# Kernel optimization log

Measured on AMD Instinct MI355X. Metric: run time of the kernel, lower is better.

The kernel has to match this reference:

```python
import jax, jax.numpy as jnp
import numpy as np

B, S, E, H = 2, 2048, 1024, 16
D = E // H  # head dim = 64
ROPE_BASE = 10000.0


def _rope(x):
    # x: [B, H, S, D]; interleaved-pair rotary embeddings (torchtune style)
    d2 = D // 2
    theta = 1.0 / (ROPE_BASE ** (jnp.arange(d2, dtype=jnp.float32) * 2.0 / D))  # [D/2]
    pos = jnp.arange(S, dtype=jnp.float32)
    ang = pos[:, None] * theta[None, :]            # [S, D/2]
    cos, sin = jnp.cos(ang), jnp.sin(ang)          # broadcast over B,H
    xr = x.reshape(B, H, S, d2, 2)
    x1, x2 = xr[..., 0], xr[..., 1]
    o1 = x1 * cos - x2 * sin
    o2 = x1 * sin + x2 * cos
    return jnp.stack([o1, o2], axis=-1).reshape(B, H, S, D)


def setup_inputs() -> dict:
    key = jax.random.key(0)
    ks = jax.random.split(key, 5)
    scale = 1.0 / np.sqrt(E)
    return {
        "x": jax.random.normal(ks[0], (B, S, E), dtype=jnp.float32),
        "Wq": jax.random.normal(ks[1], (E, E), dtype=jnp.float32) * scale,
        "Wk": jax.random.normal(ks[2], (E, E), dtype=jnp.float32) * scale,
        "Wv": jax.random.normal(ks[3], (E, E), dtype=jnp.float32) * scale,
        "Wo": jax.random.normal(ks[4], (E, E), dtype=jnp.float32) * scale,
    }


def reference(x, Wq, Wk, Wv, Wo):
    # torch Linear: y = x @ W^T
    def proj(W):
        return (x @ W.T).reshape(B, S, H, D).transpose(0, 2, 1, 3)  # [B,H,S,D]

    q = _rope(proj(Wq))
    k = _rope(proj(Wk))
    v = proj(Wv)

    attn_scale = 1.0 / np.sqrt(E)  # faithful: scales by sqrt(d_embed), not head dim
    scores = jnp.einsum('bhqd,bhkd->bhqk', q, k) * attn_scale  # [B,H,S,S]
    causal = jnp.tril(jnp.ones((S, S), dtype=bool))
    scores = jnp.where(causal, scores, -jnp.inf)
    probs = jax.nn.softmax(scores, axis=-1)
    out = jnp.einsum('bhqk,bhkd->bhqd', probs, v)  # [B,H,S,D]
    out = out.transpose(0, 2, 1, 3).reshape(B, S, E)
    return out @ Wo.T
```

## Files before the change

kernel.cpp:

```cpp
#include <hip/hip_runtime.h>
#include <hip/hip_bf16.h>
#include <math.h>

typedef __bf16 bf16;
typedef __bf16 bf16x8 __attribute__((ext_vector_type(8)));
typedef float f32x4 __attribute__((ext_vector_type(4)));

#define SEQ 2048
#define EMB 1024
#define NH  16
#define HD  64
#define NROWS 4096

#define GLOAD_LDS16(gp, lp)                                             \
    __builtin_amdgcn_global_load_lds(                                   \
        (const __attribute__((address_space(1))) void*)(gp),            \
        (__attribute__((address_space(3))) void*)(lp), 16, 0, 0)

__global__ __launch_bounds__(256) void cvt_rope_kernel(
    const float* __restrict__ x,  const float* __restrict__ Wq,
    const float* __restrict__ Wk, const float* __restrict__ Wv,
    const float* __restrict__ Wo,
    bf16* __restrict__ xb, bf16* __restrict__ Wqb, bf16* __restrict__ Wkb,
    bf16* __restrict__ Wvb, bf16* __restrict__ Wob,
    float* __restrict__ ctab, float* __restrict__ stab)
{
    int b = blockIdx.x;
    if (b >= 4096) {
        int t = (b - 4096) * 256 + threadIdx.x;
        int s = t >> 5;
        int j = t & 31;
        double freq = pow(10000.0, -(double)j / 32.0);
        double ang = (double)s * freq;
        ctab[t] = (float)cos(ang);
        stab[t] = (float)sin(ang);
        return;
    }
    const float* src; bf16* dst; int boff;
    if      (b < 2048) { src = x;  dst = xb;  boff = b;        }
    else if (b < 2560) { src = Wq; dst = Wqb; boff = b - 2048; }
    else if (b < 3072) { src = Wk; dst = Wkb; boff = b - 2560; }
    else if (b < 3584) { src = Wv; dst = Wvb; boff = b - 3072; }
    else               { src = Wo; dst = Wob; boff = b - 3584; }
    size_t off = (size_t)boff * 2048 + (size_t)threadIdx.x * 8;
    float4 f0 = *(const float4*)(src + off);
    float4 f1 = *(const float4*)(src + off + 4);
    bf16x8 v;
    v[0] = (bf16)f0.x; v[1] = (bf16)f0.y; v[2] = (bf16)f0.z; v[3] = (bf16)f0.w;
    v[4] = (bf16)f1.x; v[5] = (bf16)f1.y; v[6] = (bf16)f1.z; v[7] = (bf16)f1.w;
    *(bf16x8*)(dst + off) = v;
}

__global__ __launch_bounds__(256) void qkv_rope_kernel(
    const bf16* __restrict__ x,
    const bf16* __restrict__ Wq, const bf16* __restrict__ Wk, const bf16* __restrict__ Wv,
    const float* __restrict__ ctab, const float* __restrict__ stab,
    bf16* __restrict__ q_ws, bf16* __restrict__ kf_ws, bf16* __restrict__ vf_ws)
{
    __shared__ __align__(16) bf16 SMEM[24576];

    const int t    = threadIdx.x;
    const int lane = t & 63;
    const int wave = t >> 6;
    const int col  = lane & 15;
    const int quad = lane >> 4;

    const int nblk = blockIdx.x;
    const int m0   = blockIdx.y * 128;

    const bf16* W; int nloc;
    if (nblk < 8)       { W = Wq; nloc = nblk * 128; }
    else if (nblk < 16) { W = Wk; nloc = (nblk - 8) * 128; }
    else                { W = Wv; nloc = (nblk - 16) * 128; }

    const bf16 *ga[2], *gb[2];
#pragma unroll
    for (int j = 0; j < 2; j++) {
        int c = t + j * 256;
        ga[j] = x + (size_t)(m0 + (c >> 2)) * EMB + (c & 3) * 8;
        gb[j] = W + (size_t)(nloc + (c >> 2)) * EMB + (c & 3) * 8;
    }

    const int wm = (wave >> 1) * 64;
    const int wn = (wave & 1) * 64;

    f32x4 acc[4][4];
#pragma unroll
    for (int i = 0; i < 4; i++)
#pragma unroll
        for (int j = 0; j < 4; j++) acc[i][j] = (f32x4){0.f, 0.f, 0.f, 0.f};

    auto stage = [&](int kt, int b) {
        bf16* As_ = SMEM + b * 8192;
        bf16* Bs_ = As_ + 4096;
        const int kc = kt * 32;
#pragma unroll
        for (int j = 0; j < 2; j++) {
            const int c = t + j * 256;
            GLOAD_LDS16(ga[j] + kc, As_ + c * 8);
            GLOAD_LDS16(gb[j] + kc, Bs_ + c * 8);
        }
    };
    auto compute = [&](int b) {
        bf16* As_ = SMEM + b * 8192;
        bf16* Bs_ = As_ + 4096;
        bf16x8 a[4], bb[4];
#pragma unroll
        for (int mt = 0; mt < 4; mt++)
            a[mt] = *(const bf16x8*)(As_ + (wm + mt * 16 + col) * 32 + quad * 8);
#pragma unroll
        for (int nt = 0; nt < 4; nt++)
            bb[nt] = *(const bf16x8*)(Bs_ + (wn + nt * 16 + col) * 32 + quad * 8);
#pragma unroll
        for (int mt = 0; mt < 4; mt++)
#pragma unroll
            for (int nt = 0; nt < 4; nt++)
                acc[mt][nt] = __builtin_amdgcn_mfma_f32_16x16x32_bf16(a[mt], bb[nt], acc[mt][nt], 0, 0, 0);
    };

    stage(0, 0);
    stage(1, 1);
    int b = 0;
    for (int kt = 0; kt < 31; kt++) {
        asm volatile("s_waitcnt vmcnt(4)\n\ts_barrier" ::: "memory");
        if (kt < 30) stage(kt + 2, (kt + 2) % 3);
        compute(b);
        b = (b == 2) ? 0 : b + 1;
    }
    asm volatile("s_waitcnt vmcnt(0)\n\ts_barrier" ::: "memory");
    compute(b);
    __syncthreads();

    bf16* Es = SMEM + wave * 4608;

    const int n0w  = nblk * 128 + wn;
    const int m0w  = m0 + wm;
    const int bb_  = m0w >> 11;
    const int ss0  = m0w & (SEQ - 1);
    const int h    = (n0w >> 6) & 15;
    const int bh   = bb_ * NH + h;
    const int kind = (n0w < 1024) ? 0 : (n0w < 2048 ? 1 : 2);

#pragma unroll
    for (int mt = 0; mt < 4; mt++) {
#pragma unroll
        for (int nt = 0; nt < 4; nt++) {
            const int d  = nt * 16 + col;
            const int jj = d >> 1;
#pragma unroll
            for (int r = 0; r < 4; r++) {
                const int ss_l = mt * 16 + quad * 4 + r;
                float v = acc[mt][nt][r];
                if (kind < 2) {
                    float partner = __shfl_xor(v, 1, 64);
                    float c  = ctab[(ss0 + ss_l) * 32 + jj];
                    float sn = stab[(ss0 + ss_l) * 32 + jj];
                    float o = ((d & 1) == 0) ? (v * c - partner * sn)
                                             : (partner * sn + v * c);
                    if (kind == 0) {
                        Es[ss_l * 72 + d] = (bf16)(o * 0.03125f);
                    } else {
                        int eoff = ((ss_l >> 4) * 2 + (d >> 5)) * 512
                                 + ((d >> 3) & 3) * 128 + (ss_l & 15) * 8 + (d & 7);
                        Es[eoff] = (bf16)o;
                    }
                } else {
                    int eoff = ((ss_l >> 5) * 4 + (d >> 4)) * 512
                             + ((ss_l >> 3) & 3) * 128 + (d & 15) * 8 + (ss_l & 7);
                    Es[eoff] = (bf16)v;
                }
            }
        }
    }

    const int row = lane >> 3, c8 = lane & 7;
    if (kind == 0) {
        bf16* qbase = q_ws + ((size_t)bh * SEQ + ss0) * HD;
#pragma unroll
        for (int i = 0; i < 8; i++) {
            bf16x8 vv = *(const bf16x8*)&Es[(i * 8 + row) * 72 + c8 * 8];
            *(bf16x8*)(qbase + (size_t)(i * 8 + row) * HD + c8 * 8) = vv;
        }
    } else if (kind == 1) {
        bf16* kbase = kf_ws + ((size_t)bh * 128 + (ss0 >> 4)) * 1024;
#pragma unroll
        for (int i = 0; i < 8; i++) {
            bf16x8 vv = *(const bf16x8*)&Es[i * 512 + lane * 8];
            *(bf16x8*)(kbase + i * 512 + lane * 8) = vv;
        }
    } else {
        bf16* vbase = vf_ws + ((size_t)bh * 64 + (ss0 >> 5)) * 2048;
#pragma unroll
        for (int i = 0; i < 8; i++) {
            bf16x8 vv = *(const bf16x8*)&Es[i * 512 + lane * 8];
            *(bf16x8*)(vbase + i * 512 + lane * 8) = vv;
        }
    }
}

__global__ __launch_bounds__(128) void attn_kernel(
    const bf16* __restrict__ q_ws, const bf16* __restrict__ kf,
    const bf16* __restrict__ vf, bf16* __restrict__ attn_ws)
{
    __shared__ float comb_o[2][4][4][64];
    __shared__ float comb_l[2][64];

    const int lane = threadIdx.x & 63;
    const int wave = threadIdx.x >> 6;
    const int col  = lane & 15;
    const int quad = lane >> 4;

    const int qt = 63 - (int)(blockIdx.x >> 5);
    const int bh = blockIdx.x & 31;
    const int b_ = bh >> 4;
    const int h  = bh & 15;
    const int qb = qt * 32;
    const int nk = qt + 1;

    const bf16* Q  = q_ws + (size_t)bh * SEQ * HD;
    const bf16* Kf = kf + (size_t)bh * 131072;
    const bf16* Vf = vf + (size_t)bh * 131072;

    bf16x8 aq[2][2];
#pragma unroll
    for (int f = 0; f < 2; f++) {
        const bf16* qp = Q + (size_t)(qb + f * 16 + col) * HD + quad * 8;
        aq[f][0] = *(const bf16x8*)(qp);
        aq[f][1] = *(const bf16x8*)(qp + 32);
    }

    f32x4 acc_o[2][4];
#pragma unroll
    for (int f = 0; f < 2; f++)
#pragma unroll
        for (int i = 0; i < 4; i++) acc_o[f][i] = (f32x4){0.f, 0.f, 0.f, 0.f};
    float lsum[2] = {0.f, 0.f};

    int psrc[8];
#pragma unroll
    for (int j = 0; j < 8; j++)
        psrc[j] = ((((quad * 2 + (j >> 2)) & 3) << 4) | col) << 2;

    int s0 = (wave < nk) ? wave : 0;
    bf16x8 Ka[2][2], nKa[2][2];
    {
        const bf16* p = Kf + (size_t)s0 * 2048 + lane * 8;
        Ka[0][0] = *(const bf16x8*)(p);
        Ka[0][1] = *(const bf16x8*)(p + 512);
        Ka[1][0] = *(const bf16x8*)(p + 1024);
        Ka[1][1] = *(const bf16x8*)(p + 1536);
    }

    for (int s = wave; s < nk; s += 2) {
        bf16x8 Vb[4];
        {
            const bf16* p = Vf + (size_t)s * 2048 + lane * 8;
            Vb[0] = *(const bf16x8*)(p);
            Vb[1] = *(const bf16x8*)(p + 512);
            Vb[2] = *(const bf16x8*)(p + 1024);
            Vb[3] = *(const bf16x8*)(p + 1536);
        }

        f32x4 sT[2][2];
        __builtin_amdgcn_s_setprio(1);
#pragma unroll
        for (int g = 0; g < 2; g++)
#pragma unroll
            for (int f = 0; f < 2; f++) {
                f32x4 z = (f32x4){0.f, 0.f, 0.f, 0.f};
                z = __builtin_amdgcn_mfma_f32_16x16x32_bf16(Ka[g][0], aq[f][0], z, 0, 0, 0);
                z = __builtin_amdgcn_mfma_f32_16x16x32_bf16(Ka[g][1], aq[f][1], z, 0, 0, 0);
                sT[g][f] = z;
            }
        __builtin_amdgcn_s_setprio(0);

        {
            int sn = (s + 2 < nk) ? s + 2 : s;
            const bf16* p = Kf + (size_t)sn * 2048 + lane * 8;
            nKa[0][0] = *(const bf16x8*)(p);
            nKa[0][1] = *(const bf16x8*)(p + 512);
            nKa[1][0] = *(const bf16x8*)(p + 1024);
            nKa[1][1] = *(const bf16x8*)(p + 1536);
        }

        float p[2][2][4];
        if (s == nk - 1) {
#pragma unroll
            for (int g = 0; g < 2; g++)
#pragma unroll
                for (int f = 0; f < 2; f++) {
                    const int qg = qb + f * 16 + col;
#pragma unroll
                    for (int r = 0; r < 4; r++) {
                        int key = s * 32 + g * 16 + quad * 4 + r;
                        float e = (key <= qg) ? __expf(sT[g][f][r]) : 0.f;
                        p[g][f][r] = e;
                        lsum[f] += e;
                    }
                }
        } else {
#pragma unroll
            for (int g = 0; g < 2; g++)
#pragma unroll
                for (int f = 0; f < 2; f++)
#pragma unroll
                    for (int r = 0; r < 4; r++) {
                        float e = __expf(sT[g][f][r]);
                        p[g][f][r] = e;
                        lsum[f] += e;
                    }
        }

#pragma unroll
        for (int f = 0; f < 2; f++) {
            unsigned int pk[4];
#pragma unroll
            for (int r = 0; r < 4; r++) {
                unsigned int lo = __builtin_bit_cast(unsigned short, (bf16)p[0][f][r]);
                unsigned int hi = __builtin_bit_cast(unsigned short, (bf16)p[1][f][r]);
                pk[r] = (hi << 16) | lo;
            }
            bf16x8 a_p;
#pragma unroll
            for (int j = 0; j < 8; j++) {
                unsigned int g = (unsigned int)__builtin_amdgcn_ds_bpermute(psrc[j], (int)pk[j & 3]);
                unsigned short bits = (quad < 2) ? (unsigned short)(g & 0xffff)
                                                 : (unsigned short)(g >> 16);
                a_p[j] = __builtin_bit_cast(bf16, bits);
            }
            __builtin_amdgcn_s_setprio(1);
#pragma unroll
            for (int nt = 0; nt < 4; nt++)
                acc_o[f][nt] = __builtin_amdgcn_mfma_f32_16x16x32_bf16(a_p, Vb[nt], acc_o[f][nt], 0, 0, 0);
            __builtin_amdgcn_s_setprio(0);
        }

        Ka[0][0] = nKa[0][0]; Ka[0][1] = nKa[0][1];
        Ka[1][0] = nKa[1][0]; Ka[1][1] = nKa[1][1];
    }

    if (wave == 1) {
#pragma unroll
        for (int f = 0; f < 2; f++) {
            comb_l[f][lane] = lsum[f];
#pragma unroll
            for (int nt = 0; nt < 4; nt++)
#pragma unroll
                for (int r = 0; r < 4; r++)
                    comb_o[f][nt][r][lane] = acc_o[f][nt][r];
        }
    }
    __syncthreads();

    if (wave == 0) {
#pragma unroll
        for (int f = 0; f < 2; f++) {
            lsum[f] += comb_l[f][lane];
#pragma unroll
            for (int nt = 0; nt < 4; nt++)
#pragma unroll
                for (int r = 0; r < 4; r++)
                    acc_o[f][nt][r] += comb_o[f][nt][r][lane];
        }

#pragma unroll
        for (int f = 0; f < 2; f++) {
            lsum[f] += __shfl_xor(lsum[f], 16, 64);
            lsum[f] += __shfl_xor(lsum[f], 32, 64);
        }
#pragma unroll
        for (int f = 0; f < 2; f++)
#pragma unroll
            for (int r = 0; r < 4; r++) {
                float l_r = __shfl(lsum[f], quad * 4 + r, 64);
                float inv = 1.0f / l_r;
                int q = qb + f * 16 + quad * 4 + r;
                bf16* orow = attn_ws + (size_t)(b_ * SEQ + q) * EMB + h * HD;
#pragma unroll
                for (int nt = 0; nt < 4; nt++)
                    orow[nt * 16 + col] = (bf16)(acc_o[f][nt][r] * inv);
            }
    }
}

__global__ __launch_bounds__(256) void oproj_kernel(
    const bf16* __restrict__ attn_ws, const bf16* __restrict__ Wo,
    float* __restrict__ out)
{
    __shared__ __align__(16) bf16 SMEM[24576];

    const int t    = threadIdx.x;
    const int lane = t & 63;
    const int wave = t >> 6;
    const int col  = lane & 15;
    const int quad = lane >> 4;

    const int n0 = blockIdx.x * 128;
    const int m0 = blockIdx.y * 128;

    const bf16 *ga[2], *gb[2];
#pragma unroll
    for (int j = 0; j < 2; j++) {
        int c = t + j * 256;
        ga[j] = attn_ws + (size_t)(m0 + (c >> 2)) * EMB + (c & 3) * 8;
        gb[j] = Wo + (size_t)(n0 + (c >> 2)) * EMB + (c & 3) * 8;
    }

    const int wm = (wave >> 1) * 64;
    const int wn = (wave & 1) * 64;

    f32x4 acc[4][4];
#pragma unroll
    for (int i = 0; i < 4; i++)
#pragma unroll
        for (int j = 0; j < 4; j++) acc[i][j] = (f32x4){0.f, 0.f, 0.f, 0.f};

    auto stage = [&](int kt, int b) {
        bf16* As_ = SMEM + b * 8192;
        bf16* Bs_ = As_ + 4096;
        const int kc = kt * 32;
#pragma unroll
        for (int j = 0; j < 2; j++) {
            const int c = t + j * 256;
            GLOAD_LDS16(ga[j] + kc, As_ + c * 8);
            GLOAD_LDS16(gb[j] + kc, Bs_ + c * 8);
        }
    };
    auto compute = [&](int b) {
        bf16* As_ = SMEM + b * 8192;
        bf16* Bs_ = As_ + 4096;
        bf16x8 a[4], bb[4];
#pragma unroll
        for (int mt = 0; mt < 4; mt++)
            a[mt] = *(const bf16x8*)(As_ + (wm + mt * 16 + col) * 32 + quad * 8);
#pragma unroll
        for (int nt = 0; nt < 4; nt++)
            bb[nt] = *(const bf16x8*)(Bs_ + (wn + nt * 16 + col) * 32 + quad * 8);
#pragma unroll
        for (int mt = 0; mt < 4; mt++)
#pragma unroll
            for (int nt = 0; nt < 4; nt++)
                acc[mt][nt] = __builtin_amdgcn_mfma_f32_16x16x32_bf16(a[mt], bb[nt], acc[mt][nt], 0, 0, 0);
    };

    stage(0, 0);
    stage(1, 1);
    int b = 0;
    for (int kt = 0; kt < 31; kt++) {
        asm volatile("s_waitcnt vmcnt(4)\n\ts_barrier" ::: "memory");
        if (kt < 30) stage(kt + 2, (kt + 2) % 3);
        compute(b);
        b = (b == 2) ? 0 : b + 1;
    }
    asm volatile("s_waitcnt vmcnt(0)\n\ts_barrier" ::: "memory");
    compute(b);
    __syncthreads();

    float* Os = (float*)SMEM + (size_t)wave * 2304;
    const int row = lane >> 3, c8 = lane & 7;
    float* obase = out + (size_t)(m0 + wm) * EMB + n0 + wn;
#pragma unroll
    for (int p = 0; p < 2; p++) {
#pragma unroll
        for (int mt = 0; mt < 4; mt++)
#pragma unroll
            for (int ntl = 0; ntl < 2; ntl++)
#pragma unroll
                for (int r = 0; r < 4; r++)
                    Os[(mt * 16 + quad * 4 + r) * 36 + ntl * 16 + col] = acc[mt][p * 2 + ntl][r];
#pragma unroll
        for (int i = 0; i < 8; i++) {
            float4 vv = *(const float4*)&Os[(i * 8 + row) * 36 + c8 * 4];
            *(float4*)(obase + (size_t)(i * 8 + row) * EMB + p * 32 + c8 * 4) = vv;
        }
    }
}

extern "C" void kernel_launch(void* const* d_in, const int* in_sizes, int n_in,
                              void* d_out, int out_size, void* d_ws, size_t ws_size,
                              hipStream_t stream) {
    const float* x  = (const float*)d_in[0];
    const float* Wq = (const float*)d_in[1];
    const float* Wk = (const float*)d_in[2];
    const float* Wv = (const float*)d_in[3];
    const float* Wo = (const float*)d_in[4];
    float* out = (float*)d_out;

    char* ws = (char*)d_ws;
    bf16* q_ws    = (bf16*)(ws);
    bf16* kf_ws   = (bf16*)(ws + (8u  << 20));
    bf16* vf_ws   = (bf16*)(ws + (16u << 20));
    bf16* xb      = (bf16*)(ws + (24u << 20));
    bf16* attn_ws = (bf16*)(ws + (24u << 20));
    bf16* Wqb     = (bf16*)(ws + (32u << 20));
    bf16* Wkb     = (bf16*)(ws + (34u << 20));
    bf16* Wvb     = (bf16*)(ws + (36u << 20));
    bf16* Wob     = (bf16*)(ws + (38u << 20));
    float* ctab   = (float*)(ws + (40u << 20));
    float* stab   = ctab + SEQ * 32;

    hipLaunchKernelGGL(cvt_rope_kernel, dim3(4352), dim3(256), 0, stream,
                       x, Wq, Wk, Wv, Wo, xb, Wqb, Wkb, Wvb, Wob, ctab, stab);
    hipLaunchKernelGGL(qkv_rope_kernel, dim3(24, 32), dim3(256), 0, stream,
                       xb, Wqb, Wkb, Wvb, ctab, stab, q_ws, kf_ws, vf_ws);
    hipLaunchKernelGGL(attn_kernel, dim3(2048), dim3(128), 0, stream,
                       q_ws, kf_ws, vf_ws, attn_ws);
    hipLaunchKernelGGL(oproj_kernel, dim3(8, 32), dim3(256), 0, stream,
                       attn_ws, Wob, out);
}
```

Before: 175.6 us.

## Retile QKV GEMM to 256x256 blocks with 8 waves and swizzled LDS

The QKV projection GEMM moves from 128x128 tiles with 4 waves and a triple-buffered K=32 pipeline to 256x256 tiles with 8 waves, a double-buffered K=64 pipeline and an XOR-swizzled LDS layout. The B-tile loads are interleaved into four compute phases, and s_setprio raises wave priority around the MFMA bursts. The goal is more data reuse per LDS load, fewer LDS bank conflicts and better overlap of loads with compute. In exchange, the grid shrinks to 192 blocks, which may underfill the GPU, and register and LDS pressure rise (128KB LDS per block).

```diff
diff --git a/kernel.cpp b/kernel.cpp
--- a/kernel.cpp
+++ b/kernel.cpp
@@ -51,149 +51,177 @@
     *(bf16x8*)(dst + off) = v;
 }
 
-__global__ __launch_bounds__(256) void qkv_rope_kernel(
+__global__ __launch_bounds__(512, 2) void qkv_rope_kernel(
     const bf16* __restrict__ x,
     const bf16* __restrict__ Wq, const bf16* __restrict__ Wk, const bf16* __restrict__ Wv,
     const float* __restrict__ ctab, const float* __restrict__ stab,
     bf16* __restrict__ q_ws, bf16* __restrict__ kf_ws, bf16* __restrict__ vf_ws)
 {
-    __shared__ __align__(16) bf16 SMEM[24576];
+    __shared__ __align__(16) bf16 SMEM[65536];
 
     const int t    = threadIdx.x;
     const int lane = t & 63;
     const int wave = t >> 6;
     const int col  = lane & 15;
     const int quad = lane >> 4;
+    const int wmi  = wave >> 2;
+    const int wni  = wave & 3;
 
     const int nblk = blockIdx.x;
-    const int m0   = blockIdx.y * 128;
-
-    const bf16* W; int nloc;
-    if (nblk < 8)       { W = Wq; nloc = nblk * 128; }
-    else if (nblk < 16) { W = Wk; nloc = (nblk - 8) * 128; }
-    else                { W = Wv; nloc = (nblk - 16) * 128; }
-
-    const bf16 *ga[2], *gb[2];
-#pragma unroll
-    for (int j = 0; j < 2; j++) {
-        int c = t + j * 256;
-        ga[j] = x + (size_t)(m0 + (c >> 2)) * EMB + (c & 3) * 8;
-        gb[j] = W + (size_t)(nloc + (c >> 2)) * EMB + (c & 3) * 8;
-    }
-
-    const int wm = (wave >> 1) * 64;
-    const int wn = (wave & 1) * 64;
-
-    f32x4 acc[4][4];
-#pragma unroll
-    for (int i = 0; i < 4; i++)
+    const int m0   = blockIdx.y * 256;
+
+    const bf16* W;
+    const int nloc = (nblk & 3) * 256;
+    if (nblk < 4)      W = Wq;
+    else if (nblk < 8) W = Wk;
+    else               W = Wv;
+
+    const int srow = t >> 3;
+    const int scol = ((t & 7) ^ (srow & 7)) * 8;
+    const bf16* gaA = x + (size_t)(m0   + srow) * EMB + scol;
+    const bf16* gaB = W + (size_t)(nloc + srow) * EMB + scol;
+
+    f32x4 acc[8][4];
+#pragma unroll
+    for (int i = 0; i < 8; i++)
 #pragma unroll
         for (int j = 0; j < 4; j++) acc[i][j] = (f32x4){0.f, 0.f, 0.f, 0.f};
 
-    auto stage = [&](int kt, int b) {
-        bf16* As_ = SMEM + b * 8192;
-        bf16* Bs_ = As_ + 4096;
-        const int kc = kt * 32;
-#pragma unroll
-        for (int j = 0; j < 2; j++) {
-            const int c = t + j * 256;
-            GLOAD_LDS16(ga[j] + kc, As_ + c * 8);
-            GLOAD_LDS16(gb[j] + kc, Bs_ + c * 8);
-        }
+    auto stageA = [&](int kt, int h) {
+        bf16* dst = SMEM + (kt & 1) * 32768 + h * 8192 + t * 8;
+        const bf16* src = gaA + (size_t)(h * 128) * EMB + kt * 64;
+        GLOAD_LDS16(src,            dst);
+        GLOAD_LDS16(src + 64 * EMB, dst + 4096);
     };
-    auto compute = [&](int b) {
-        bf16* As_ = SMEM + b * 8192;
-        bf16* Bs_ = As_ + 4096;
-        bf16x8 a[4], bb[4];
-#pragma unroll
-        for (int mt = 0; mt < 4; mt++)
-            a[mt] = *(const bf16x8*)(As_ + (wm + mt * 16 + col) * 32 + quad * 8);
-#pragma unroll
-        for (int nt = 0; nt < 4; nt++)
-            bb[nt] = *(const bf16x8*)(Bs_ + (wn + nt * 16 + col) * 32 + quad * 8);
-#pragma unroll
-        for (int mt = 0; mt < 4; mt++)
-#pragma unroll
-            for (int nt = 0; nt < 4; nt++)
-                acc[mt][nt] = __builtin_amdgcn_mfma_f32_16x16x32_bf16(a[mt], bb[nt], acc[mt][nt], 0, 0, 0);
+    auto stageB = [&](int kt, int h) {
+        bf16* dst = SMEM + (kt & 1) * 32768 + 16384 + h * 8192 + t * 8;
+        const bf16* src = gaB + (size_t)(h * 128) * EMB + kt * 64;
+        GLOAD_LDS16(src,            dst);
+        GLOAD_LDS16(src + 64 * EMB, dst + 4096);
     };
 
-    stage(0, 0);
-    stage(1, 1);
-    int b = 0;
-    for (int kt = 0; kt < 31; kt++) {
-        asm volatile("s_waitcnt vmcnt(4)\n\ts_barrier" ::: "memory");
-        if (kt < 30) stage(kt + 2, (kt + 2) % 3);
-        compute(b);
-        b = (b == 2) ? 0 : b + 1;
-    }
-    asm volatile("s_waitcnt vmcnt(0)\n\ts_barrier" ::: "memory");
-    compute(b);
+    const int swz = (col & 7) << 3;
+
+    auto phase = [&](int p, int mh, int nh, int skt, int sh) {
+        const bf16* Ab = SMEM + p * 32768;
+        const bf16* Bb = SMEM + p * 32768 + 16384;
+        bf16x8 a[4][2], b[2][2];
+#pragma unroll
+        for (int mtl = 0; mtl < 4; mtl++) {
+            const int row = wmi * 128 + mh * 64 + mtl * 16 + col;
+#pragma unroll
+            for (int kk = 0; kk < 2; kk++)
+                a[mtl][kk] = *(const bf16x8*)(Ab + row * 64 + ((quad * 8 + kk * 32) ^ swz));
+        }
+#pragma unroll
+        for (int ntl = 0; ntl < 2; ntl++) {
+            const int row = wni * 64 + nh * 32 + ntl * 16 + col;
+#pragma unroll
+            for (int kk = 0; kk < 2; kk++)
+                b[ntl][kk] = *(const bf16x8*)(Bb + row * 64 + ((quad * 8 + kk * 32) ^ swz));
+        }
+        if (skt >= 0) stageB(skt, sh);
+        __builtin_amdgcn_s_setprio(1);
+#pragma unroll
+        for (int mtl = 0; mtl < 4; mtl++)
+#pragma unroll
+            for (int ntl = 0; ntl < 2; ntl++) {
+                f32x4 c = acc[mh * 4 + mtl][nh * 2 + ntl];
+                c = __builtin_amdgcn_mfma_f32_16x16x32_bf16(a[mtl][0], b[ntl][0], c, 0, 0, 0);
+                c = __builtin_amdgcn_mfma_f32_16x16x32_bf16(a[mtl][1], b[ntl][1], c, 0, 0, 0);
+                acc[mh * 4 + mtl][nh * 2 + ntl] = c;
+            }
+        __builtin_amdgcn_s_setprio(0);
+        __builtin_amdgcn_s_barrier();
+    };
+
+    stageA(0, 0); stageA(0, 1); stageB(0, 0); stageB(0, 1);
+
+    for (int kt = 0; kt < 15; kt++) {
+        const int p = kt & 1;
+        stageA(kt + 1, 0); stageA(kt + 1, 1);
+        asm volatile("s_waitcnt vmcnt(4)" ::: "memory");
+        __builtin_amdgcn_s_barrier();
+        phase(p, 0, 0, kt + 1, 0);
+        phase(p, 0, 1, kt + 1, 1);
+        phase(p, 1, 0, -1, 0);
+        phase(p, 1, 1, -1, 0);
+    }
+    asm volatile("s_waitcnt vmcnt(0)" ::: "memory");
+    __builtin_amdgcn_s_barrier();
+    phase(1, 0, 0, -1, 0);
+    phase(1, 0, 1, -1, 0);
+    phase(1, 1, 0, -1, 0);
+    phase(1, 1, 1, -1, 0);
     __syncthreads();
 
     bf16* Es = SMEM + wave * 4608;
 
-    const int n0w  = nblk * 128 + wn;
-    const int m0w  = m0 + wm;
-    const int bb_  = m0w >> 11;
-    const int ss0  = m0w & (SEQ - 1);
-    const int h    = (n0w >> 6) & 15;
-    const int bh   = bb_ * NH + h;
+    const int n0w  = nblk * 256 + wni * 64;
+    const int hd_  = (n0w >> 6) & 15;
     const int kind = (n0w < 1024) ? 0 : (n0w < 2048 ? 1 : 2);
-
-#pragma unroll
-    for (int mt = 0; mt < 4; mt++) {
-#pragma unroll
-        for (int nt = 0; nt < 4; nt++) {
-            const int d  = nt * 16 + col;
-            const int jj = d >> 1;
-#pragma unroll
-            for (int r = 0; r < 4; r++) {
-                const int ss_l = mt * 16 + quad * 4 + r;
-                float v = acc[mt][nt][r];
-                if (kind < 2) {
-                    float partner = __shfl_xor(v, 1, 64);
-                    float c  = ctab[(ss0 + ss_l) * 32 + jj];
-                    float sn = stab[(ss0 + ss_l) * 32 + jj];
-                    float o = ((d & 1) == 0) ? (v * c - partner * sn)
-                                             : (partner * sn + v * c);
-                    if (kind == 0) {
-                        Es[ss_l * 72 + d] = (bf16)(o * 0.03125f);
+    const int row8 = lane >> 3, c8 = lane & 7;
+
+#pragma unroll
+    for (int P = 0; P < 2; P++) {
+        const int m0w = m0 + wmi * 128 + P * 64;
+        const int bb_ = m0w >> 11;
+        const int ss0 = m0w & (SEQ - 1);
+        const int bh  = bb_ * NH + hd_;
+
+#pragma unroll
+        for (int mtl = 0; mtl < 4; mtl++) {
+#pragma unroll
+            for (int nt = 0; nt < 4; nt++) {
+                const int d  = nt * 16 + col;
+                const int jj = d >> 1;
+#pragma unroll
+                for (int r = 0; r < 4; r++) {
+                    const int ss_l = mtl * 16 + quad * 4 + r;
+                    float v = acc[P * 4 + mtl][nt][r];
+                    if (kind < 2) {
+                        float partner = __shfl_xor(v, 1, 64);
+                        float c  = ctab[(ss0 + ss_l) * 32 + jj];
+                        float sn = stab[(ss0 + ss_l) * 32 + jj];
+                        float o = ((d & 1) == 0) ? (v * c - partner * sn)
+                                                 : (partner * sn + v * c);
+                        if (kind == 0) {
+                            Es[ss_l * 72 + d] = (bf16)(o * 0.03125f);
+                        } else {
+                            int eoff = ((ss_l >> 4) * 2 + (d >> 5)) * 512
+                                     + ((d >> 3) & 3) * 128 + (ss_l & 15) * 8 + (d & 7);
+                            Es[eoff] = (bf16)o;
+                        }
                     } else {
-                        int eoff = ((ss_l >> 4) * 2 + (d >> 5)) * 512
-                                 + ((d >> 3) & 3) * 128 + (ss_l & 15) * 8 + (d & 7);
-                        Es[eoff] = (bf16)o;
+                        int eoff = ((ss_l >> 5) * 4 + (d >> 4)) * 512
+                                 + ((ss_l >> 3) & 3) * 128 + (d & 15) * 8 + (ss_l & 7);
+                        Es[eoff] = (bf16)v;
                     }
-                } else {
-                    int eoff = ((ss_l >> 5) * 4 + (d >> 4)) * 512
-                             + ((ss_l >> 3) & 3) * 128 + (d & 15) * 8 + (ss_l & 7);
-                    Es[eoff] = (bf16)v;
                 }
             }
         }
-    }
-
-    const int row = lane >> 3, c8 = lane & 7;
-    if (kind == 0) {
-        bf16* qbase = q_ws + ((size_t)bh * SEQ + ss0) * HD;
-#pragma unroll
-        for (int i = 0; i < 8; i++) {
-            bf16x8 vv = *(const bf16x8*)&Es[(i * 8 + row) * 72 + c8 * 8];
-            *(bf16x8*)(qbase + (size_t)(i * 8 + row) * HD + c8 * 8) = vv;
-        }
-    } else if (kind == 1) {
-        bf16* kbase = kf_ws + ((size_t)bh * 128 + (ss0 >> 4)) * 1024;
-#pragma unroll
-        for (int i = 0; i < 8; i++) {
-            bf16x8 vv = *(const bf16x8*)&Es[i * 512 + lane * 8];
-            *(bf16x8*)(kbase + i * 512 + lane * 8) = vv;
-        }
-    } else {
-        bf16* vbase = vf_ws + ((size_t)bh * 64 + (ss0 >> 5)) * 2048;
-#pragma unroll
-        for (int i = 0; i < 8; i++) {
-            bf16x8 vv = *(const bf16x8*)&Es[i * 512 + lane * 8];
-            *(bf16x8*)(vbase + i * 512 + lane * 8) = vv;
+
+        if (kind == 0) {
+            bf16* qbase = q_ws + ((size_t)bh * SEQ + ss0) * HD;
+#pragma unroll
+            for (int i = 0; i < 8; i++) {
+                bf16x8 vv = *(const bf16x8*)&Es[(i * 8 + row8) * 72 + c8 * 8];
+                *(bf16x8*)(qbase + (size_t)(i * 8 + row8) * HD + c8 * 8) = vv;
+            }
+        } else if (kind == 1) {
+            bf16* kbase = kf_ws + ((size_t)bh * 128 + (ss0 >> 4)) * 1024;
+#pragma unroll
+            for (int i = 0; i < 8; i++) {
+                bf16x8 vv = *(const bf16x8*)&Es[i * 512 + lane * 8];
+                *(bf16x8*)(kbase + i * 512 + lane * 8) = vv;
+            }
+        } else {
+            bf16* vbase = vf_ws + ((size_t)bh * 64 + (ss0 >> 5)) * 2048;
+#pragma unroll
+            for (int i = 0; i < 8; i++) {
+                bf16x8 vv = *(const bf16x8*)&Es[i * 512 + lane * 8];
+                *(bf16x8*)(vbase + i * 512 + lane * 8) = vv;
+            }
         }
     }
 }
@@ -501,7 +529,7 @@
 
     hipLaunchKernelGGL(cvt_rope_kernel, dim3(4352), dim3(256), 0, stream,
                        x, Wq, Wk, Wv, Wo, xb, Wqb, Wkb, Wvb, Wob, ctab, stab);
-    hipLaunchKernelGGL(qkv_rope_kernel, dim3(24, 32), dim3(256), 0, stream,
+    hipLaunchKernelGGL(qkv_rope_kernel, dim3(12, 16), dim3(512), 0, stream,
                        xb, Wqb, Wkb, Wvb, ctab, stab, q_ws, kf_ws, vf_ws);
     hipLaunchKernelGGL(attn_kernel, dim3(2048), dim3(128), 0, stream,
                        q_ws, kf_ws, vf_ws, attn_ws);
```

After: 190.0 us. +8.2%, slower.

## Fuse fp32-to-bf16 conversion and RoPE table into GEMM kernels

Applied to the files above, without the earlier changes.

Removes the separate conversion/RoPE-table kernel. The QKV and output-projection GEMMs now read fp32 operands directly, convert them to bf16 in registers, and write them to LDS through a double buffer. The QKV kernel also computes the per-block cos/sin table in shared memory with fast intrinsics after range reduction. This saves a kernel launch and the extra bf16 round trip through global memory. In exchange it drops the async global-to-LDS three-stage pipeline, reads twice as many bytes per tile, and raises LDS use in the QKV kernel, which may cut occupancy.

```diff
diff --git a/kernel.cpp b/kernel.cpp
--- a/kernel.cpp
+++ b/kernel.cpp
@@ -10,54 +10,27 @@
 #define EMB 1024
 #define NH  16
 #define HD  64
-#define NROWS 4096
 
 #define GLOAD_LDS16(gp, lp)                                             \
     __builtin_amdgcn_global_load_lds(                                   \
         (const __attribute__((address_space(1))) void*)(gp),            \
         (__attribute__((address_space(3))) void*)(lp), 16, 0, 0)
 
-__global__ __launch_bounds__(256) void cvt_rope_kernel(
-    const float* __restrict__ x,  const float* __restrict__ Wq,
-    const float* __restrict__ Wk, const float* __restrict__ Wv,
-    const float* __restrict__ Wo,
-    bf16* __restrict__ xb, bf16* __restrict__ Wqb, bf16* __restrict__ Wkb,
-    bf16* __restrict__ Wvb, bf16* __restrict__ Wob,
-    float* __restrict__ ctab, float* __restrict__ stab)
-{
-    int b = blockIdx.x;
-    if (b >= 4096) {
-        int t = (b - 4096) * 256 + threadIdx.x;
-        int s = t >> 5;
-        int j = t & 31;
-        double freq = pow(10000.0, -(double)j / 32.0);
-        double ang = (double)s * freq;
-        ctab[t] = (float)cos(ang);
-        stab[t] = (float)sin(ang);
-        return;
-    }
-    const float* src; bf16* dst; int boff;
-    if      (b < 2048) { src = x;  dst = xb;  boff = b;        }
-    else if (b < 2560) { src = Wq; dst = Wqb; boff = b - 2048; }
-    else if (b < 3072) { src = Wk; dst = Wkb; boff = b - 2560; }
-    else if (b < 3584) { src = Wv; dst = Wvb; boff = b - 3072; }
-    else               { src = Wo; dst = Wob; boff = b - 3584; }
-    size_t off = (size_t)boff * 2048 + (size_t)threadIdx.x * 8;
-    float4 f0 = *(const float4*)(src + off);
-    float4 f1 = *(const float4*)(src + off + 4);
+__device__ __forceinline__ bf16x8 cvt8(const float4& f0, const float4& f1) {
     bf16x8 v;
     v[0] = (bf16)f0.x; v[1] = (bf16)f0.y; v[2] = (bf16)f0.z; v[3] = (bf16)f0.w;
     v[4] = (bf16)f1.x; v[5] = (bf16)f1.y; v[6] = (bf16)f1.z; v[7] = (bf16)f1.w;
-    *(bf16x8*)(dst + off) = v;
+    return v;
 }
 
 __global__ __launch_bounds__(256) void qkv_rope_kernel(
-    const bf16* __restrict__ x,
-    const bf16* __restrict__ Wq, const bf16* __restrict__ Wk, const bf16* __restrict__ Wv,
-    const float* __restrict__ ctab, const float* __restrict__ stab,
+    const float* __restrict__ x,
+    const float* __restrict__ Wq, const float* __restrict__ Wk, const float* __restrict__ Wv,
     bf16* __restrict__ q_ws, bf16* __restrict__ kf_ws, bf16* __restrict__ vf_ws)
 {
-    __shared__ __align__(16) bf16 SMEM[24576];
+    __shared__ __align__(16) char SM[69632];
+    float* tabc = (float*)(SM + 36864);
+    float* tabs = (float*)(SM + 53248);
 
     const int t    = threadIdx.x;
     const int lane = t & 63;
@@ -68,17 +41,17 @@
     const int nblk = blockIdx.x;
     const int m0   = blockIdx.y * 128;
 
-    const bf16* W; int nloc;
+    const float* W; int nloc;
     if (nblk < 8)       { W = Wq; nloc = nblk * 128; }
     else if (nblk < 16) { W = Wk; nloc = (nblk - 8) * 128; }
     else                { W = Wv; nloc = (nblk - 16) * 128; }
 
-    const bf16 *ga[2], *gb[2];
+    const float *gA[2], *gB[2];
 #pragma unroll
     for (int j = 0; j < 2; j++) {
         int c = t + j * 256;
-        ga[j] = x + (size_t)(m0 + (c >> 2)) * EMB + (c & 3) * 8;
-        gb[j] = W + (size_t)(nloc + (c >> 2)) * EMB + (c & 3) * 8;
+        gA[j] = x + (size_t)(m0   + (c >> 2)) * EMB + (c & 3) * 8;
+        gB[j] = W + (size_t)(nloc + (c >> 2)) * EMB + (c & 3) * 8;
     }
 
     const int wm = (wave >> 1) * 64;
@@ -90,20 +63,30 @@
 #pragma unroll
         for (int j = 0; j < 4; j++) acc[i][j] = (f32x4){0.f, 0.f, 0.f, 0.f};
 
-    auto stage = [&](int kt, int b) {
-        bf16* As_ = SMEM + b * 8192;
-        bf16* Bs_ = As_ + 4096;
+    float4 rA[2][2], rB[2][2];
+    auto issue = [&](int kt) {
         const int kc = kt * 32;
 #pragma unroll
         for (int j = 0; j < 2; j++) {
-            const int c = t + j * 256;
-            GLOAD_LDS16(ga[j] + kc, As_ + c * 8);
-            GLOAD_LDS16(gb[j] + kc, Bs_ + c * 8);
+            rA[j][0] = *(const float4*)(gA[j] + kc);
+            rA[j][1] = *(const float4*)(gA[j] + kc + 4);
+            rB[j][0] = *(const float4*)(gB[j] + kc);
+            rB[j][1] = *(const float4*)(gB[j] + kc + 4);
         }
     };
-    auto compute = [&](int b) {
-        bf16* As_ = SMEM + b * 8192;
-        bf16* Bs_ = As_ + 4096;
+    auto write_buf = [&](int p) {
+        bf16* As_ = (bf16*)(SM + p * 16384);
+        bf16* Bs_ = (bf16*)(SM + p * 16384 + 8192);
+#pragma unroll
+        for (int j = 0; j < 2; j++) {
+            int c = t + j * 256;
+            *(bf16x8*)(As_ + c * 8) = cvt8(rA[j][0], rA[j][1]);
+            *(bf16x8*)(Bs_ + c * 8) = cvt8(rB[j][0], rB[j][1]);
+        }
+    };
+    auto compute = [&](int p) {
+        const bf16* As_ = (const bf16*)(SM + p * 16384);
+        const bf16* Bs_ = (const bf16*)(SM + p * 16384 + 8192);
         bf16x8 a[4], bb[4];
 #pragma unroll
         for (int mt = 0; mt < 4; mt++)
@@ -118,20 +101,37 @@
                 acc[mt][nt] = __builtin_amdgcn_mfma_f32_16x16x32_bf16(a[mt], bb[nt], acc[mt][nt], 0, 0, 0);
     };
 
-    stage(0, 0);
-    stage(1, 1);
-    int b = 0;
-    for (int kt = 0; kt < 31; kt++) {
-        asm volatile("s_waitcnt vmcnt(4)\n\ts_barrier" ::: "memory");
-        if (kt < 30) stage(kt + 2, (kt + 2) % 3);
-        compute(b);
-        b = (b == 2) ? 0 : b + 1;
-    }
-    asm volatile("s_waitcnt vmcnt(0)\n\ts_barrier" ::: "memory");
-    compute(b);
+    issue(0);
+
+    {
+        const int sbase = m0 & (SEQ - 1);
+        const double TWOPI = 6.283185307179586476;
+        const double INV2PI = 0.15915494309189533577;
+#pragma unroll
+        for (int i = 0; i < 16; i++) {
+            int idx = t * 16 + i;
+            int row = idx >> 5;
+            int jj  = idx & 31;
+            float freq = exp2f((float)jj * -0.4152410118609203f);
+            double a = (double)(sbase + row) * (double)freq;
+            double n = floor(a * INV2PI);
+            float red = (float)(a - n * TWOPI);
+            tabc[idx] = __cosf(red);
+            tabs[idx] = __sinf(red);
+        }
+    }
+
+    for (int kt = 0; kt < 32; kt++) {
+        const int p = kt & 1;
+        asm volatile("s_waitcnt vmcnt(0)" ::: "memory");
+        write_buf(p);
+        __syncthreads();
+        if (kt < 31) issue(kt + 1);
+        compute(p);
+    }
     __syncthreads();
 
-    bf16* Es = SMEM + wave * 4608;
+    bf16* Es = (bf16*)SM + wave * 4608;
 
     const int n0w  = nblk * 128 + wn;
     const int m0w  = m0 + wm;
@@ -153,8 +153,9 @@
                 float v = acc[mt][nt][r];
                 if (kind < 2) {
                     float partner = __shfl_xor(v, 1, 64);
-                    float c  = ctab[(ss0 + ss_l) * 32 + jj];
-                    float sn = stab[(ss0 + ss_l) * 32 + jj];
+                    const int ti = (wm + ss_l) * 32 + jj;
+                    float c  = tabc[ti];
+                    float sn = tabs[ti];
                     float o = ((d & 1) == 0) ? (v * c - partner * sn)
                                              : (partner * sn + v * c);
                     if (kind == 0) {
@@ -384,10 +385,10 @@
 }
 
 __global__ __launch_bounds__(256) void oproj_kernel(
-    const bf16* __restrict__ attn_ws, const bf16* __restrict__ Wo,
+    const bf16* __restrict__ attn_ws, const float* __restrict__ Wo,
     float* __restrict__ out)
 {
-    __shared__ __align__(16) bf16 SMEM[24576];
+    __shared__ __align__(16) char SM[36864];
 
     const int t    = threadIdx.x;
     const int lane = t & 63;
@@ -398,12 +399,13 @@
     const int n0 = blockIdx.x * 128;
     const int m0 = blockIdx.y * 128;
 
-    const bf16 *ga[2], *gb[2];
+    const bf16  *gA[2];
+    const float *gB[2];
 #pragma unroll
     for (int j = 0; j < 2; j++) {
         int c = t + j * 256;
-        ga[j] = attn_ws + (size_t)(m0 + (c >> 2)) * EMB + (c & 3) * 8;
-        gb[j] = Wo + (size_t)(n0 + (c >> 2)) * EMB + (c & 3) * 8;
+        gA[j] = attn_ws + (size_t)(m0 + (c >> 2)) * EMB + (c & 3) * 8;
+        gB[j] = Wo + (size_t)(n0 + (c >> 2)) * EMB + (c & 3) * 8;
     }
 
     const int wm = (wave >> 1) * 64;
@@ -415,20 +417,28 @@
 #pragma unroll
         for (int j = 0; j < 4; j++) acc[i][j] = (f32x4){0.f, 0.f, 0.f, 0.f};
 
-    auto stage = [&](int kt, int b) {
-        bf16* As_ = SMEM + b * 8192;
-        bf16* Bs_ = As_ + 4096;
+    float4 rB[2][2];
+    auto issue = [&](int kt) {
         const int kc = kt * 32;
 #pragma unroll
         for (int j = 0; j < 2; j++) {
-            const int c = t + j * 256;
-            GLOAD_LDS16(ga[j] + kc, As_ + c * 8);
-            GLOAD_LDS16(gb[j] + kc, Bs_ + c * 8);
+            int c = t + j * 256;
+            GLOAD_LDS16(gA[j] + kc, (bf16*)(SM + ((kt & 1) * 16384)) + c * 8);
+            rB[j][0] = *(const float4*)(gB[j] + kc);
+            rB[j][1] = *(const float4*)(gB[j] + kc + 4);
         }
     };
-    auto compute = [&](int b) {
-        bf16* As_ = SMEM + b * 8192;
-        bf16* Bs_ = As_ + 4096;
+    auto write_buf = [&](int p) {
+        bf16* Bs_ = (bf16*)(SM + p * 16384 + 8192);
+#pragma unroll
+        for (int j = 0; j < 2; j++) {
+            int c = t + j * 256;
+            *(bf16x8*)(Bs_ + c * 8) = cvt8(rB[j][0], rB[j][1]);
+        }
+    };
+    auto compute = [&](int p) {
+        const bf16* As_ = (const bf16*)(SM + p * 16384);
+        const bf16* Bs_ = (const bf16*)(SM + p * 16384 + 8192);
         bf16x8 a[4], bb[4];
 #pragma unroll
         for (int mt = 0; mt < 4; mt++)
@@ -443,20 +453,18 @@
                 acc[mt][nt] = __builtin_amdgcn_mfma_f32_16x16x32_bf16(a[mt], bb[nt], acc[mt][nt], 0, 0, 0);
     };
 
-    stage(0, 0);
-    stage(1, 1);
-    int b = 0;
-    for (int kt = 0; kt < 31; kt++) {
-        asm volatile("s_waitcnt vmcnt(4)\n\ts_barrier" ::: "memory");
-        if (kt < 30) stage(kt + 2, (kt + 2) % 3);
-        compute(b);
-        b = (b == 2) ? 0 : b + 1;
-    }
-    asm volatile("s_waitcnt vmcnt(0)\n\ts_barrier" ::: "memory");
-    compute(b);
+    issue(0);
+    for (int kt = 0; kt < 32; kt++) {
+        const int p = kt & 1;
+        asm volatile("s_waitcnt vmcnt(0)" ::: "memory");
+        write_buf(p);
+        __syncthreads();
+        if (kt < 31) issue(kt + 1);
+        compute(p);
+    }
     __syncthreads();
 
-    float* Os = (float*)SMEM + (size_t)wave * 2304;
+    float* Os = (float*)(SM + (size_t)wave * 9216);
     const int row = lane >> 3, c8 = lane & 7;
     float* obase = out + (size_t)(m0 + wm) * EMB + n0 + wn;
 #pragma unroll
@@ -490,21 +498,12 @@
     bf16* q_ws    = (bf16*)(ws);
     bf16* kf_ws   = (bf16*)(ws + (8u  << 20));
     bf16* vf_ws   = (bf16*)(ws + (16u << 20));
-    bf16* xb      = (bf16*)(ws + (24u << 20));
     bf16* attn_ws = (bf16*)(ws + (24u << 20));
-    bf16* Wqb     = (bf16*)(ws + (32u << 20));
-    bf16* Wkb     = (bf16*)(ws + (34u << 20));
-    bf16* Wvb     = (bf16*)(ws + (36u << 20));
-    bf16* Wob     = (bf16*)(ws + (38u << 20));
-    float* ctab   = (float*)(ws + (40u << 20));
-    float* stab   = ctab + SEQ * 32;
-
-    hipLaunchKernelGGL(cvt_rope_kernel, dim3(4352), dim3(256), 0, stream,
-                       x, Wq, Wk, Wv, Wo, xb, Wqb, Wkb, Wvb, Wob, ctab, stab);
+
     hipLaunchKernelGGL(qkv_rope_kernel, dim3(24, 32), dim3(256), 0, stream,
-                       xb, Wqb, Wkb, Wvb, ctab, stab, q_ws, kf_ws, vf_ws);
+                       x, Wq, Wk, Wv, q_ws, kf_ws, vf_ws);
     hipLaunchKernelGGL(attn_kernel, dim3(2048), dim3(128), 0, stream,
                        q_ws, kf_ws, vf_ws, attn_ws);
     hipLaunchKernelGGL(oproj_kernel, dim3(8, 32), dim3(256), 0, stream,
-                       attn_ws, Wob, out);
+                       attn_ws, Wo, out);
 }
```

New measurement: 218.5 us. 24.4% more time.
